# Kernel optimization log

Hardware: AMD Instinct MI355X
Metric: run time of the kernel (lower is better)

## Reference

```python
import jax, jax.numpy as jnp
import numpy as np

TOP_K = 2
EPS = 1e-10


def setup_inputs() -> dict:
    key = jax.random.key(0)
    k1, k2 = jax.random.split(key)
    B, S, D, E = 4, 4096, 4096, 64
    hidden_states = jax.random.normal(k1, (B, S, D), dtype=jnp.float32)
    # router weight, scaled like a standard linear init
    w_router = jax.random.normal(k2, (D, E), dtype=jnp.float32) / np.sqrt(D)
    return {"hidden_states": hidden_states, "w_router": w_router}


def reference(hidden_states, w_router):
    # router: [B,S,D] x [D,E] -> [B,S,E]
    router_logits = jnp.einsum("bsd,de->bse", hidden_states, w_router)
    # balanced_assignment: softmax, global load, penalty, adjusted top-k
    routing_probs = jax.nn.softmax(router_logits, axis=-1)
    current_load = routing_probs.sum(axis=(0, 1))            # [E]
    load_penalty = current_load / (current_load.mean() + EPS)  # [E]
    adjusted_logits = router_logits - jnp.log(load_penalty + EPS)
    _, expert_indices = jax.lax.top_k(adjusted_logits, TOP_K)  # [B,S,top_k]
    return adjusted_logits, expert_indices
```

## Files before the change

### kernel.cpp

```cpp
#include <hip/hip_runtime.h>
#include <math.h>

#define ROWS 16384
#define DD   4096
#define EE   64
#define EPSF 1e-10f

#define BM     64
#define KSPLIT 2
#define KRANGE (DD / KSPLIT)
#define KT     64
#define NPH    (KRANGE / KT)
#define WTILE  8192
#define BTILE  (2 * WTILE)

typedef __attribute__((ext_vector_type(8))) short short8;
typedef __attribute__((ext_vector_type(4))) float f32x4;
typedef __attribute__((ext_vector_type(4))) unsigned u32x4;

__device__ __forceinline__ void split2x8(const float f[8], u32x4& w0,
                                         u32x4& w1) {
#pragma unroll
  for (int i = 0; i < 4; ++i) {
    float fa = f[2 * i], fb = f[2 * i + 1];
    unsigned ua = __float_as_uint(fa), ub = __float_as_uint(fb);
    unsigned ra = ua + 0x7fffu + ((ua >> 16) & 1u);
    unsigned rb = ub + 0x7fffu + ((ub >> 16) & 1u);
    w0[i] = (rb & 0xffff0000u) | (ra >> 16);
    fa -= __uint_as_float(ra & 0xffff0000u);
    fb -= __uint_as_float(rb & 0xffff0000u);
    ua = __float_as_uint(fa); ub = __float_as_uint(fb);
    ra = ua + 0x7fffu + ((ua >> 16) & 1u);
    rb = ub + 0x7fffu + ((ub >> 16) & 1u);
    w1[i] = (rb & 0xffff0000u) | (ra >> 16);
  }
}

__device__ __forceinline__ void dma16(const void* g, void* l) {
  __builtin_amdgcn_global_load_lds(
      (const __attribute__((address_space(1))) unsigned int*)g,
      (__attribute__((address_space(3))) unsigned int*)l, 16, 0, 0);
}

__global__ __launch_bounds__(256) void k_wsplit(const float* __restrict__ wr,
                                                unsigned char* __restrict__ out,
                                                float* __restrict__ g_load) {
  const int kt = blockIdx.x;
  const int t = threadIdx.x;
  const int lane = t & 63, wv = t >> 6;
  if (blockIdx.x == 0 && t < 64) g_load[t] = 0.f;
  float f[8];
  const float* wp = wr + (size_t)(kt * 32 + wv * 8) * EE + lane;
#pragma unroll
  for (int j = 0; j < 8; ++j) f[j] = wp[(size_t)j * EE];
  u32x4 w0, w1;
  split2x8(f, w0, w1);
  const int et = lane >> 4;
  const int lp = wv * 16 + (lane & 15);
  unsigned char* base = out + (size_t)kt * WTILE + et * 1024 + lp * 16;
  *(u32x4*)(base + 0 * 4096) = w0;
  *(u32x4*)(base + 1 * 4096) = w1;
}

__global__ __launch_bounds__(512) void k_gemm(
    const float* __restrict__ h, const unsigned char* __restrict__ wsp,
    float* __restrict__ logits) {
  __shared__ alignas(16) unsigned char smem[2 * BTILE];

  const int t = threadIdx.x;
  const int lane = t & 63;
  const int wv = t >> 6;
  const int mt = wv >> 1;
  const int sub = wv & 1;
  const int row0 = (blockIdx.x >> 1) * BM;
  const int ks = blockIdx.x & 1;

  f32x4 acc[4] = {};

  const float* ap = h + (size_t)(row0 + mt * 16 + (lane & 15)) * DD +
                    ks * KRANGE + sub * 32 + (lane >> 4) * 8;
  const unsigned char* wbase = wsp + (size_t)ks * NPH * BTILE;
  const int dmaoff = t * 16;

  float4 c0, c1, n0, n1;

#pragma unroll
  for (int i = 0; i < 2; ++i)
    dma16(wbase + i * 8192 + dmaoff, smem + i * 8192 + dmaoff);
  c0 = *(const float4*)(ap);
  c1 = *(const float4*)(ap + 4);

  for (int kt = 0; kt < NPH; ++kt) {
    const int buf = kt & 1;
    asm volatile("s_waitcnt vmcnt(0)" ::: "memory");
    __syncthreads();

    if (kt + 1 < NPH) {
      const unsigned char* ws = wbase + (size_t)(kt + 1) * BTILE;
      unsigned char* nb = smem + (buf ^ 1) * BTILE;
#pragma unroll
      for (int i = 0; i < 2; ++i)
        dma16(ws + i * 8192 + dmaoff, nb + i * 8192 + dmaoff);
      const float* p = ap + (size_t)(kt + 1) * KT;
      n0 = *(const float4*)(p);
      n1 = *(const float4*)(p + 4);
    }

    const unsigned char* lb = smem + buf * BTILE + sub * WTILE;
    short8 bf[2][4];
#pragma unroll
    for (int p = 0; p < 2; ++p)
#pragma unroll
      for (int e = 0; e < 4; ++e)
        bf[p][e] = *(const short8*)&lb[p * 4096 + e * 1024 + lane * 16];

    const float af[8] = {c0.x, c0.y, c0.z, c0.w, c1.x, c1.y, c1.z, c1.w};
    u32x4 q0, q1;
    split2x8(af, q0, q1);
    const short8 ah0 = __builtin_bit_cast(short8, q0);
    const short8 ah1 = __builtin_bit_cast(short8, q1);
#pragma unroll
    for (int e = 0; e < 4; ++e) {
      f32x4 c = acc[e];
      c = __builtin_amdgcn_mfma_f32_16x16x32_bf16(ah0, bf[0][e], c, 0, 0, 0);
      c = __builtin_amdgcn_mfma_f32_16x16x32_bf16(ah0, bf[1][e], c, 0, 0, 0);
      c = __builtin_amdgcn_mfma_f32_16x16x32_bf16(ah1, bf[0][e], c, 0, 0, 0);
      acc[e] = c;
    }

    if (kt + 1 < NPH) { c0 = n0; c1 = n1; }
  }

  const int rbase = row0 + mt * 16 + (lane >> 4) * 4;
  const int col = lane & 15;
#pragma unroll
  for (int e = 0; e < 4; ++e)
#pragma unroll
    for (int r = 0; r < 4; ++r)
      atomicAdd(&logits[(size_t)(rbase + r) * EE + e * 16 + col],
                acc[e][r]);
}

__global__ __launch_bounds__(256) void k_softload(
    const float* __restrict__ logits, float* __restrict__ g_load) {
  __shared__ float red[4][64];
  const int lane = threadIdx.x & 63;
  const int wv = threadIdx.x >> 6;
  float accp = 0.f;
#pragma unroll 4
  for (int i = 0; i < 16; ++i) {
    int row = blockIdx.x * 64 + wv * 16 + i;
    float x = logits[(size_t)row * EE + lane];
    float m = x;
#pragma unroll
    for (int off = 32; off > 0; off >>= 1) m = fmaxf(m, __shfl_xor(m, off, 64));
    float p = __expf(x - m);
    float s = p;
#pragma unroll
    for (int off = 32; off > 0; off >>= 1) s += __shfl_xor(s, off, 64);
    accp += p / s;
  }
  red[wv][lane] = accp;
  __syncthreads();
  if (wv == 0) {
    float s = red[0][lane] + red[1][lane] + red[2][lane] + red[3][lane];
    atomicAdd(&g_load[lane], s);
  }
}

__global__ __launch_bounds__(256) void k_top2(float* __restrict__ logits,
                                              const float* __restrict__ g_load,
                                              float* __restrict__ idx_out) {
  int t = threadIdx.x;
  int lane = t & 63;
  int wv = t >> 6;
  int row = blockIdx.x * 4 + wv;

  float v0 = g_load[lane];
  float s0 = v0;
#pragma unroll
  for (int off = 32; off > 0; off >>= 1) s0 += __shfl_xor(s0, off, 64);
  float lp = logf(v0 / (s0 * (1.f / 64.f) + EPSF) + EPSF);

  size_t base = (size_t)row * EE;
  float a = logits[base + lane] - lp;
  logits[base + lane] = a;

  float v = a;
  int idx = lane;
#pragma unroll
  for (int off = 32; off > 0; off >>= 1) {
    float ov = __shfl_xor(v, off, 64);
    int oi = __shfl_xor(idx, off, 64);
    if (ov > v || (ov == v && oi < idx)) { v = ov; idx = oi; }
  }
  int i1 = idx;

  float a2 = (lane == i1) ? -INFINITY : a;
  v = a2;
  idx = lane;
#pragma unroll
  for (int off = 32; off > 0; off >>= 1) {
    float ov = __shfl_xor(v, off, 64);
    int oi = __shfl_xor(idx, off, 64);
    if (ov > v || (ov == v && oi < idx)) { v = ov; idx = oi; }
  }
  int i2 = idx;

  if (lane == 0) {
    idx_out[(size_t)row * 2 + 0] = (float)i1;
    idx_out[(size_t)row * 2 + 1] = (float)i2;
  }
}

extern "C" void kernel_launch(void* const* d_in, const int* in_sizes, int n_in,
                              void* d_out, int out_size, void* d_ws,
                              size_t ws_size, hipStream_t stream) {
  const float* h = (const float*)d_in[0];
  const float* wr = (const float*)d_in[1];
  float* out = (float*)d_out;
  float* logits = out;
  float* idx_out = out + (size_t)ROWS * EE;
  float* g_load = (float*)d_ws;
  unsigned char* wsp = (unsigned char*)d_ws + 512;

  hipMemsetAsync(logits, 0, (size_t)ROWS * EE * sizeof(float), stream);
  k_wsplit<<<DD / 32, 256, 0, stream>>>(wr, wsp, g_load);
  k_gemm<<<(ROWS / BM) * KSPLIT, 512, 0, stream>>>(h, wsp, logits);
  k_softload<<<ROWS / 64, 256, 0, stream>>>(logits, g_load);
  k_top2<<<ROWS / 4, 256, 0, stream>>>(logits, g_load, idx_out);
}
```

Measured before the change: 404.6 us.

## Fold logits zeroing into weight-split kernel and halve GEMM block threads

The separate memset of the logits buffer is removed, and its zeroing moves into the weight-split kernel: each of its 128 blocks clears 2048 float4s. The GEMM block shrinks from 8 to 4 waves. Each wave now covers both K-subhalves of the 64-wide K tile in a loop, so it loads twice as many A values per step and does twice the MFMA work. This drops a launch and raises per-wave register use and serial work, while occupancy and latency hiding may change.

```diff
diff --git a/kernel.cpp b/kernel.cpp
--- a/kernel.cpp
+++ b/kernel.cpp
@@ -44,11 +44,18 @@
 
 __global__ __launch_bounds__(256) void k_wsplit(const float* __restrict__ wr,
                                                 unsigned char* __restrict__ out,
+                                                float* __restrict__ logits,
                                                 float* __restrict__ g_load) {
   const int kt = blockIdx.x;
   const int t = threadIdx.x;
   const int lane = t & 63, wv = t >> 6;
   if (blockIdx.x == 0 && t < 64) g_load[t] = 0.f;
+  {
+    float4 z = {0.f, 0.f, 0.f, 0.f};
+    float4* lp4 = (float4*)logits + (size_t)blockIdx.x * 2048 + t;
+#pragma unroll
+    for (int i = 0; i < 8; ++i) lp4[i * 256] = z;
+  }
   float f[8];
   const float* wp = wr + (size_t)(kt * 32 + wv * 8) * EE + lane;
 #pragma unroll
@@ -62,7 +69,7 @@
   *(u32x4*)(base + 1 * 4096) = w1;
 }
 
-__global__ __launch_bounds__(512) void k_gemm(
+__global__ __launch_bounds__(256) void k_gemm(
     const float* __restrict__ h, const unsigned char* __restrict__ wsp,
     float* __restrict__ logits) {
   __shared__ alignas(16) unsigned char smem[2 * BTILE];
@@ -70,25 +77,25 @@
   const int t = threadIdx.x;
   const int lane = t & 63;
   const int wv = t >> 6;
-  const int mt = wv >> 1;
-  const int sub = wv & 1;
   const int row0 = (blockIdx.x >> 1) * BM;
   const int ks = blockIdx.x & 1;
 
   f32x4 acc[4] = {};
 
-  const float* ap = h + (size_t)(row0 + mt * 16 + (lane & 15)) * DD +
-                    ks * KRANGE + sub * 32 + (lane >> 4) * 8;
+  const float* ap = h + (size_t)(row0 + wv * 16 + (lane & 15)) * DD +
+                    ks * KRANGE + (lane >> 4) * 8;
   const unsigned char* wbase = wsp + (size_t)ks * NPH * BTILE;
   const int dmaoff = t * 16;
 
-  float4 c0, c1, n0, n1;
-
-#pragma unroll
-  for (int i = 0; i < 2; ++i)
-    dma16(wbase + i * 8192 + dmaoff, smem + i * 8192 + dmaoff);
+  float4 c0, c1, c2, c3, n0, n1, n2, n3;
+
+#pragma unroll
+  for (int i = 0; i < 4; ++i)
+    dma16(wbase + i * 4096 + dmaoff, smem + i * 4096 + dmaoff);
   c0 = *(const float4*)(ap);
   c1 = *(const float4*)(ap + 4);
+  c2 = *(const float4*)(ap + 32);
+  c3 = *(const float4*)(ap + 36);
 
   for (int kt = 0; kt < NPH; ++kt) {
     const int buf = kt & 1;
@@ -99,39 +106,47 @@
       const unsigned char* ws = wbase + (size_t)(kt + 1) * BTILE;
       unsigned char* nb = smem + (buf ^ 1) * BTILE;
 #pragma unroll
-      for (int i = 0; i < 2; ++i)
-        dma16(ws + i * 8192 + dmaoff, nb + i * 8192 + dmaoff);
+      for (int i = 0; i < 4; ++i)
+        dma16(ws + i * 4096 + dmaoff, nb + i * 4096 + dmaoff);
       const float* p = ap + (size_t)(kt + 1) * KT;
       n0 = *(const float4*)(p);
       n1 = *(const float4*)(p + 4);
+      n2 = *(const float4*)(p + 32);
+      n3 = *(const float4*)(p + 36);
     }
 
-    const unsigned char* lb = smem + buf * BTILE + sub * WTILE;
-    short8 bf[2][4];
-#pragma unroll
-    for (int p = 0; p < 2; ++p)
-#pragma unroll
-      for (int e = 0; e < 4; ++e)
-        bf[p][e] = *(const short8*)&lb[p * 4096 + e * 1024 + lane * 16];
-
-    const float af[8] = {c0.x, c0.y, c0.z, c0.w, c1.x, c1.y, c1.z, c1.w};
-    u32x4 q0, q1;
-    split2x8(af, q0, q1);
-    const short8 ah0 = __builtin_bit_cast(short8, q0);
-    const short8 ah1 = __builtin_bit_cast(short8, q1);
-#pragma unroll
-    for (int e = 0; e < 4; ++e) {
-      f32x4 c = acc[e];
-      c = __builtin_amdgcn_mfma_f32_16x16x32_bf16(ah0, bf[0][e], c, 0, 0, 0);
-      c = __builtin_amdgcn_mfma_f32_16x16x32_bf16(ah0, bf[1][e], c, 0, 0, 0);
-      c = __builtin_amdgcn_mfma_f32_16x16x32_bf16(ah1, bf[0][e], c, 0, 0, 0);
-      acc[e] = c;
+    const unsigned char* lb = smem + buf * BTILE;
+#pragma unroll
+    for (int sub = 0; sub < 2; ++sub) {
+      const unsigned char* sb = lb + sub * WTILE;
+      short8 bf[2][4];
+#pragma unroll
+      for (int p = 0; p < 2; ++p)
+#pragma unroll
+        for (int e = 0; e < 4; ++e)
+          bf[p][e] = *(const short8*)&sb[p * 4096 + e * 1024 + lane * 16];
+
+      const float4 a0 = sub ? c2 : c0;
+      const float4 a1 = sub ? c3 : c1;
+      const float af[8] = {a0.x, a0.y, a0.z, a0.w, a1.x, a1.y, a1.z, a1.w};
+      u32x4 q0, q1;
+      split2x8(af, q0, q1);
+      const short8 ah0 = __builtin_bit_cast(short8, q0);
+      const short8 ah1 = __builtin_bit_cast(short8, q1);
+#pragma unroll
+      for (int e = 0; e < 4; ++e) {
+        f32x4 c = acc[e];
+        c = __builtin_amdgcn_mfma_f32_16x16x32_bf16(ah0, bf[0][e], c, 0, 0, 0);
+        c = __builtin_amdgcn_mfma_f32_16x16x32_bf16(ah0, bf[1][e], c, 0, 0, 0);
+        c = __builtin_amdgcn_mfma_f32_16x16x32_bf16(ah1, bf[0][e], c, 0, 0, 0);
+        acc[e] = c;
+      }
     }
 
-    if (kt + 1 < NPH) { c0 = n0; c1 = n1; }
-  }
-
-  const int rbase = row0 + mt * 16 + (lane >> 4) * 4;
+    if (kt + 1 < NPH) { c0 = n0; c1 = n1; c2 = n2; c3 = n3; }
+  }
+
+  const int rbase = row0 + wv * 16 + (lane >> 4) * 4;
   const int col = lane & 15;
 #pragma unroll
   for (int e = 0; e < 4; ++e)
@@ -224,9 +239,8 @@
   float* g_load = (float*)d_ws;
   unsigned char* wsp = (unsigned char*)d_ws + 512;
 
-  hipMemsetAsync(logits, 0, (size_t)ROWS * EE * sizeof(float), stream);
-  k_wsplit<<<DD / 32, 256, 0, stream>>>(wr, wsp, g_load);
-  k_gemm<<<(ROWS / BM) * KSPLIT, 512, 0, stream>>>(h, wsp, logits);
+  k_wsplit<<<DD / 32, 256, 0, stream>>>(wr, wsp, logits, g_load);
+  k_gemm<<<(ROWS / BM) * KSPLIT, 256, 0, stream>>>(h, wsp, logits);
   k_softload<<<ROWS / 64, 256, 0, stream>>>(logits, g_load);
   k_top2<<<ROWS / 4, 256, 0, stream>>>(logits, g_load, idx_out);
 }
```

Result: no change. 400.0 us (-1.1%).
